# Kernel optimization log

Measured on AMD Instinct MI355X. Metric: run time of the kernel, lower is better.

Reference implementation:

```python
import jax, jax.numpy as jnp
import numpy as np

N = 50000      # nodes
E = 400000     # edges
IN = 128       # in_channels
C = 32         # out_channels per head
H1 = 8         # heads layer 1
MSG = 64       # msg_dim
TD = 64        # time encoder out_channels
ED = MSG + TD  # edge_dim = 128
HID = H1 * C   # 256


def _lin(k, fi, fo):
    return jax.random.normal(k, (fi, fo), jnp.float32) / np.float32(np.sqrt(fi))


def setup_inputs() -> dict:
    key = jax.random.key(0)
    ks = jax.random.split(key, 32)
    inp = {
        'x': jax.random.normal(ks[0], (N, IN), jnp.float32),
        'last_update': jax.random.uniform(ks[1], (N,), jnp.float32) * 1000.0,
        'edge_index': jax.random.randint(ks[2], (2, E), 0, N, jnp.int64),
        't': jax.random.uniform(ks[3], (E,), jnp.float32) * 1000.0,
        'msg': jax.random.normal(ks[4], (E, MSG), jnp.float32),
        # time encoder: Linear(1, TD) then cos
        'tw': jax.random.normal(ks[5], (TD,), jnp.float32),
        'tb': jnp.zeros((TD,), jnp.float32),
        # layer 1: TransformerConv(IN, C, heads=8, concat=True, edge_dim=ED)
        'Wq1': _lin(ks[6], IN, HID), 'bq1': jnp.zeros((HID,), jnp.float32),
        'Wk1': _lin(ks[7], IN, HID), 'bk1': jnp.zeros((HID,), jnp.float32),
        'Wv1': _lin(ks[8], IN, HID), 'bv1': jnp.zeros((HID,), jnp.float32),
        'We1': _lin(ks[9], ED, HID),                       # lin_edge, no bias
        'Ws1': _lin(ks[10], IN, HID), 'bs1': jnp.zeros((HID,), jnp.float32),
        # layer 2: TransformerConv(HID, C, heads=1, concat=False, edge_dim=ED)
        'Wq2': _lin(ks[11], HID, C), 'bq2': jnp.zeros((C,), jnp.float32),
        'Wk2': _lin(ks[12], HID, C), 'bk2': jnp.zeros((C,), jnp.float32),
        'Wv2': _lin(ks[13], HID, C), 'bv2': jnp.zeros((C,), jnp.float32),
        'We2': _lin(ks[14], ED, C),
        'Ws2': _lin(ks[15], HID, C), 'bs2': jnp.zeros((C,), jnp.float32),
    }
    return inp


def _seg_softmax(logits, seg, n):
    # numerically-stable softmax over variable-size neighborhoods (per dst node)
    m = jax.ops.segment_max(logits, seg, num_segments=n)
    m = jnp.where(jnp.isfinite(m), m, 0.0)
    e = jnp.exp(logits - jax.lax.stop_gradient(m)[seg])
    s = jax.ops.segment_sum(e, seg, num_segments=n)
    return e / (s[seg] + 1e-16)


def _transformer_conv(x, edge_attr, src, dst, Wq, bq, Wk, bk, Wv, bv, We, Ws, bs, heads, ch, concat):
    n = x.shape[0]
    q = (x @ Wq + bq).reshape(n, heads, ch)[dst]          # (E,H,C) gather at dst
    k = ((x @ Wk + bk)[src]).reshape(-1, heads, ch)       # (E,H,C) gather at src
    v = ((x @ Wv + bv)[src]).reshape(-1, heads, ch)
    e = (edge_attr @ We).reshape(-1, heads, ch)
    k = k + e
    alpha = (q * k).sum(-1) / np.float32(np.sqrt(ch))     # (E,H)
    alpha = _seg_softmax(alpha, dst, n)
    out = jax.ops.segment_sum(alpha[..., None] * (v + e), dst, num_segments=n)  # (N,H,C)
    out = out.reshape(n, heads * ch) if concat else out.mean(axis=1)
    return out + x @ Ws + bs                               # root/skip connection


def reference(x, last_update, edge_index, t, msg, tw, tb,
              Wq1, bq1, Wk1, bk1, Wv1, bv1, We1, Ws1, bs1,
              Wq2, bq2, Wk2, bk2, Wv2, bv2, We2, Ws2, bs2):
    src, dst = edge_index[0], edge_index[1]
    rel_t = last_update[src] - t                          # (E,)
    rel_enc = jnp.cos(rel_t[:, None] * tw[None, :] + tb)  # TGN time encoding (E,TD)
    edge_attr = jnp.concatenate([rel_enc, msg], axis=-1)  # (E,ED)
    h = jax.nn.relu(_transformer_conv(x, edge_attr, src, dst,
                                      Wq1, bq1, Wk1, bk1, Wv1, bv1, We1, Ws1, bs1,
                                      H1, C, True))
    out = jax.nn.relu(_transformer_conv(h, edge_attr, src, dst,
                                        Wq2, bq2, Wk2, bk2, Wv2, bv2, We2, Ws2, bs2,
                                        1, C, False))
    return out
```

## Files before the change

kernel.cpp:

```cpp
#include <hip/hip_runtime.h>
#include <math.h>

#define NN 50000
#define NE 400000
#define RSQRT32 0.17677669529663687f

typedef __attribute__((ext_vector_type(8))) short bf16x8;
typedef __attribute__((ext_vector_type(4))) float f32x4;
#define MFMA_B16(a, b, c) __builtin_amdgcn_mfma_f32_16x16x32_bf16(a, b, c, 0, 0, 0)

#define O_FLAG  0ULL
#define O_BSUM  256ULL
#define O_SRCI  1280ULL
#define O_DSTI  (O_SRCI + 1600000ULL)
#define O_DEG   (O_DSTI + 1600000ULL)
#define O_CUR   (O_DEG + 200192ULL)
#define O_START (O_CUR + 200192ULL)
#define O_SRCS  (O_START + 200704ULL)
#define O_ORIG  (O_SRCS + 1600000ULL)
#define O_RELT  (O_ORIG + 1600000ULL)
#define O_Q1    (O_RELT + 1600000ULL)
#define O_K1    (O_Q1 + 25600000ULL)
#define O_V1    (O_K1 + 25600000ULL)
#define O_S1M   (O_V1 + 25600000ULL)
#define O_G1    (O_S1M + 25600000ULL)
#define O_WB1   (O_G1 + 102400000ULL)
#define O_WG1   (O_WB1 + 262144ULL)
#define O_WF1   (O_WG1 + 65536ULL)
#define O_WB2   (O_WF1 + 65536ULL)
#define O_NUMV1 (O_WB2 + 65536ULL)
#define WS_TOTAL (O_NUMV1 + 51200000ULL)
#define O_S1    O_DSTI
#define O_A1    O_G1
#define O_H     O_V1
#define O_Q2    O_Q1
#define O_K2    (O_Q1 + 6400000ULL)
#define O_V2    (O_Q1 + 12800000ULL)
#define O_S2M   (O_Q1 + 19200000ULL)
#define O_G2    O_K1
#define O_A2    O_S1M
#define O_NUMV2 O_G1
#define O_S2    O_CUR

__device__ __forceinline__ unsigned short f2bf(float f) {
    unsigned int u = __float_as_uint(f);
    unsigned int r = (u + 0x7fffu + ((u >> 16) & 1u)) >> 16;
    return (unsigned short)r;
}
__device__ __forceinline__ float bf2f(unsigned short u) {
    return __uint_as_float(((unsigned int)u) << 16);
}
__device__ __forceinline__ float4 ld_bf16x4(const unsigned short* p) {
    const ushort4 u = *(const ushort4*)p;
    float4 r;
    r.x = bf2f(u.x); r.y = bf2f(u.y); r.z = bf2f(u.z); r.w = bf2f(u.w);
    return r;
}
__device__ __forceinline__ ushort4 st_bf16x4(float a, float b, float c, float d) {
    ushort4 u; u.x = f2bf(a); u.y = f2bf(b); u.z = f2bf(c); u.w = f2bf(d);
    return u;
}

__global__ void k_detect(const unsigned int* ei, int* flag) {
    if (threadIdx.x == 0) {
        int is64 = 1;
        for (int i = 0; i < 64; ++i)
            if (ei[2 * i + 1] != 0u) { is64 = 0; break; }
        *flag = is64;
    }
}

__global__ void k_convhist(const void* ei, const int* flag,
                           int* __restrict__ srcI, int* __restrict__ dstI,
                           int* __restrict__ deg) {
    int i = blockIdx.x * 256 + threadIdx.x;
    if (i >= NE) return;
    int s, d;
    if (*flag) {
        const long long* p = (const long long*)ei;
        s = (int)p[i]; d = (int)p[NE + i];
    } else {
        const int* p = (const int*)ei;
        s = p[i]; d = p[NE + i];
    }
    srcI[i] = s;
    dstI[i] = d;
    atomicAdd(&deg[d], 1);
}

__global__ void k_scanA(const int* __restrict__ deg, int* __restrict__ locs,
                        int* __restrict__ bsum) {
    __shared__ int sm[256];
    const int t = threadIdx.x;
    const int gidx = blockIdx.x * 256 + t;
    int v = (gidx < NN) ? deg[gidx] : 0;
    sm[t] = v;
    __syncthreads();
    for (int off = 1; off < 256; off <<= 1) {
        int u = (t >= off) ? sm[t - off] : 0;
        __syncthreads();
        sm[t] += u;
        __syncthreads();
    }
    if (gidx < NN) locs[gidx] = sm[t];
    if (t == 255) bsum[blockIdx.x] = sm[255];
}

__global__ void k_scanB(int* __restrict__ bsum) {
    __shared__ int sm[256];
    const int t = threadIdx.x;
    int v = (t < 196) ? bsum[t] : 0;
    sm[t] = v;
    __syncthreads();
    for (int off = 1; off < 256; off <<= 1) {
        int u = (t >= off) ? sm[t - off] : 0;
        __syncthreads();
        sm[t] += u;
        __syncthreads();
    }
    if (t < 196) bsum[t] = sm[t] - v;
}

__global__ void k_scanC(const int* __restrict__ deg, const int* __restrict__ bsum,
                        int* __restrict__ startA, int* __restrict__ cursor) {
    const int t = threadIdx.x;
    const int gidx = blockIdx.x * 256 + t;
    if (gidx < NN) {
        const int ex = startA[gidx] - deg[gidx] + bsum[blockIdx.x];
        startA[gidx] = ex;
        cursor[gidx] = ex;
    }
    if (gidx == 0) startA[NN] = NE;
}

__global__ void k_scatter(const int* __restrict__ srcI, const int* __restrict__ dstI,
                          const float* __restrict__ lu, const float* __restrict__ tE,
                          int* __restrict__ cursor,
                          int* __restrict__ srcS, int* __restrict__ orig,
                          float* __restrict__ relT) {
    int i = blockIdx.x * 256 + threadIdx.x;
    if (i >= NE) return;
    const int d = dstI[i];
    const int s = srcI[i];
    const int pos = atomicAdd(&cursor[d], 1);
    srcS[pos] = s;
    orig[pos] = i;
    relT[pos] = lu[s] - tE[i];
}

__global__ void k_prepw(
    const float* __restrict__ Wq1, const float* __restrict__ Wk1,
    const float* __restrict__ Wv1, const float* __restrict__ Ws1,
    const float* __restrict__ We1,
    const float* __restrict__ Wq2, const float* __restrict__ Wk2,
    const float* __restrict__ Wv2, const float* __restrict__ Ws2,
    unsigned short* __restrict__ WB1, unsigned short* __restrict__ WG1,
    unsigned short* __restrict__ WF1, unsigned short* __restrict__ WB2)
{
    const int i = blockIdx.x * 256 + threadIdx.x;
    if (i < 131072) {
        const int part = i >> 15;
        const int rem = i & 32767;
        const int n = rem >> 7, k = rem & 127;
        const float* W = part == 0 ? Wq1 : part == 1 ? Wk1 : part == 2 ? Wv1 : Ws1;
        WB1[i] = f2bf(W[(size_t)k * 256 + n]);
    } else if (i < 163840) {
        const int j = i - 131072;
        const int h = j >> 12, ko = (j >> 5) & 127, c = j & 31;
        WG1[j] = f2bf(We1[(size_t)ko * 256 + h * 32 + c]);
    } else if (i < 196608) {
        const int j = i - 163840;
        const int h = j >> 12, c = (j >> 7) & 31, ko = j & 127;
        WF1[j] = f2bf(We1[(size_t)ko * 256 + h * 32 + c]);
    } else if (i < 229376) {
        const int j = i - 196608;
        const int col = j >> 8, k = j & 255;
        const int part = col >> 5, pc = col & 31;
        const float* W = part == 0 ? Wq2 : part == 1 ? Wk2 : part == 2 ? Wv2 : Ws2;
        WB2[j] = f2bf(W[(size_t)k * 32 + pc]);
    }
}

__global__ __launch_bounds__(256) void k_gemm1m(
    const float* __restrict__ x, const unsigned short* __restrict__ WB1,
    const float* __restrict__ c0, const float* __restrict__ c1,
    const float* __restrict__ c2, const float* __restrict__ c3,
    unsigned short* __restrict__ Q1b, unsigned short* __restrict__ K1b,
    unsigned short* __restrict__ V1b, unsigned short* __restrict__ S1mb)
{
    __shared__ unsigned short As[64 * 136];
    __shared__ unsigned short Bs[64 * 136];
    const int t = threadIdx.x;
    const int row0 = blockIdx.x * 64;
    const int by = blockIdx.y;
    const int part = by >> 2;
    const int pcol0 = (by & 3) * 64;
    const float* bp = part == 0 ? c0 : part == 1 ? c1 : part == 2 ? c2 : c3;
    unsigned short* Ob = part == 0 ? Q1b : part == 1 ? K1b : part == 2 ? V1b : S1mb;

    {
        const int r = t >> 2, cc = (t & 3) * 32;
        const int gr = row0 + r;
        unsigned short* dst = As + r * 136 + cc;
        if (gr < NN) {
            const float4* xp = (const float4*)(x + (size_t)gr * 128 + cc);
            #pragma unroll
            for (int i = 0; i < 8; ++i) {
                const float4 v = xp[i];
                *(ushort4*)(dst + 4 * i) = st_bf16x4(v.x, v.y, v.z, v.w);
            }
        } else {
            const ushort4 z = {0, 0, 0, 0};
            #pragma unroll
            for (int i = 0; i < 8; ++i) *(ushort4*)(dst + 4 * i) = z;
        }
    }
    {
        const int n = t >> 2, kk = (t & 3) * 32;
        const unsigned short* src = WB1 + ((size_t)part * 256 + pcol0 + n) * 128 + kk;
        unsigned short* dst = Bs + n * 136 + kk;
        #pragma unroll
        for (int i = 0; i < 4; ++i)
            *(bf16x8*)(dst + 8 * i) = *(const bf16x8*)(src + 8 * i);
    }
    __syncthreads();

    const int w = t >> 6, lane = t & 63, m = lane & 15, quad = lane >> 4;
    f32x4 acc[4];
    #pragma unroll
    for (int i = 0; i < 4; ++i) acc[i] = (f32x4){0.f, 0.f, 0.f, 0.f};
    #pragma unroll
    for (int kc = 0; kc < 4; ++kc) {
        const bf16x8 af = *(const bf16x8*)(As + (16 * w + m) * 136 + kc * 32 + quad * 8);
        #pragma unroll
        for (int ct = 0; ct < 4; ++ct) {
            const bf16x8 bf = *(const bf16x8*)(Bs + (16 * ct + m) * 136 + kc * 32 + quad * 8);
            acc[ct] = MFMA_B16(af, bf, acc[ct]);
        }
    }
    #pragma unroll
    for (int ct = 0; ct < 4; ++ct) {
        const int colp = pcol0 + ct * 16 + m;
        const float b = bp[colp];
        #pragma unroll
        for (int r = 0; r < 4; ++r) {
            const int gr = row0 + 16 * w + quad * 4 + r;
            if (gr < NN) Ob[(size_t)gr * 256 + colp] = f2bf(acc[ct][r] + b);
        }
    }
}

__global__ __launch_bounds__(256) void k_g1m(
    const unsigned short* __restrict__ Q1b, const unsigned short* __restrict__ WG1,
    unsigned short* __restrict__ G1b)
{
    __shared__ unsigned short As[64 * 40];
    __shared__ unsigned short Bs[128 * 40];
    const int t = threadIdx.x;
    const int n0 = blockIdx.x * 64;
    const int h = blockIdx.y;
    {
        const int n = t >> 2, c = (t & 3) * 8;
        const int gn = n0 + n;
        bf16x8 v = {};
        if (gn < NN) v = *(const bf16x8*)(Q1b + (size_t)gn * 256 + h * 32 + c);
        *(bf16x8*)(As + n * 40 + c) = v;
    }
    {
        const int ko = t >> 1, c = (t & 1) * 16;
        const unsigned short* src = WG1 + (size_t)h * 4096 + ko * 32 + c;
        *(bf16x8*)(Bs + ko * 40 + c) = *(const bf16x8*)(src);
        *(bf16x8*)(Bs + ko * 40 + c + 8) = *(const bf16x8*)(src + 8);
    }
    __syncthreads();

    const int w = t >> 6, lane = t & 63, m = lane & 15, quad = lane >> 4;
    f32x4 acc[8];
    #pragma unroll
    for (int i = 0; i < 8; ++i) acc[i] = (f32x4){0.f, 0.f, 0.f, 0.f};
    const bf16x8 af = *(const bf16x8*)(As + (16 * w + m) * 40 + quad * 8);
    #pragma unroll
    for (int ct = 0; ct < 8; ++ct) {
        const bf16x8 bf = *(const bf16x8*)(Bs + (16 * ct + m) * 40 + quad * 8);
        acc[ct] = MFMA_B16(af, bf, acc[ct]);
    }
    #pragma unroll
    for (int ct = 0; ct < 8; ++ct) {
        const int k = ct * 16 + m;
        #pragma unroll
        for (int r = 0; r < 4; ++r) {
            const int gn = n0 + 16 * w + quad * 4 + r;
            if (gn < NN) G1b[(size_t)gn * 1024 + h * 128 + k] = f2bf(acc[ct][r]);
        }
    }
}

__global__ __launch_bounds__(256) void k_g2(
    const float* __restrict__ Q2, const float* __restrict__ We2,
    float* __restrict__ G2)
{
    __shared__ float Qs[64][36];
    __shared__ float Ws[128][36];
    const int t = threadIdx.x;
    const int n0 = blockIdx.x * 64;
    {
        const int n = t >> 2, c8 = (t & 3) * 8;
        float4 v0 = make_float4(0.f,0.f,0.f,0.f), v1 = v0;
        if (n0 + n < NN) {
            v0 = *(const float4*)(Q2 + (size_t)(n0 + n) * 32 + c8);
            v1 = *(const float4*)(Q2 + (size_t)(n0 + n) * 32 + c8 + 4);
        }
        *(float4*)(&Qs[n][c8]) = v0;
        *(float4*)(&Qs[n][c8 + 4]) = v1;
    }
    {
        const int k = t >> 1, c16 = (t & 1) * 16;
        #pragma unroll
        for (int i = 0; i < 4; ++i)
            *(float4*)(&Ws[k][c16 + 4 * i]) =
                *(const float4*)(We2 + (size_t)k * 32 + c16 + 4 * i);
    }
    __syncthreads();
    const int tx = t & 15, ty = t >> 4;
    const int k8 = tx * 8, n4 = ty * 4;
    float acc[4][8] = {};
    #pragma unroll 8
    for (int c = 0; c < 32; ++c) {
        float a[4], b[8];
        #pragma unroll
        for (int i = 0; i < 4; ++i) a[i] = Qs[n4 + i][c];
        #pragma unroll
        for (int j = 0; j < 8; ++j) b[j] = Ws[k8 + j][c];
        #pragma unroll
        for (int i = 0; i < 4; ++i)
            #pragma unroll
            for (int j = 0; j < 8; ++j)
                acc[i][j] += a[i] * b[j];
    }
    #pragma unroll
    for (int i = 0; i < 4; ++i) {
        const int gn = n0 + n4 + i;
        if (gn < NN) {
            float* gp = G2 + (size_t)gn * 128 + k8;
            *(float4*)(gp)     = make_float4(acc[i][0], acc[i][1], acc[i][2], acc[i][3]);
            *(float4*)(gp + 4) = make_float4(acc[i][4], acc[i][5], acc[i][6], acc[i][7]);
        }
    }
}

__global__ __launch_bounds__(256) __attribute__((amdgpu_waves_per_eu(3)))
void k_agg1(
    const int* __restrict__ startA, const int* __restrict__ srcS,
    const int* __restrict__ orig, const float* __restrict__ relT,
    const float* __restrict__ msg, const float* __restrict__ tw,
    const float* __restrict__ tb,
    const unsigned short* __restrict__ Q1b, const unsigned short* __restrict__ K1b,
    const unsigned short* __restrict__ V1b, const unsigned short* G1b,
    unsigned short* A1b, float* __restrict__ numv1, float* __restrict__ s1)
{
    const int t = threadIdx.x;
    const int g = t >> 5, l = t & 31;
    const int lane64 = t & 63;
    const int base32 = lane64 & 32;
    const int d = blockIdx.x * 8 + g;
    const int eb = startA[d], ee = startA[d + 1];
    const int hl = l >> 2;

    float q8[8];
    {
        const unsigned short* qp = Q1b + (size_t)d * 256 + l * 8;
        const float4 q0 = ld_bf16x4(qp), q1 = ld_bf16x4(qp + 4);
        q8[0]=q0.x; q8[1]=q0.y; q8[2]=q0.z; q8[3]=q0.w;
        q8[4]=q1.x; q8[5]=q1.y; q8[6]=q1.z; q8[7]=q1.w;
    }
    float gv[8][4];
    #pragma unroll
    for (int h = 0; h < 8; ++h) {
        const float4 gg = ld_bf16x4(G1b + (size_t)d * 1024 + h * 128 + l * 4);
        gv[h][0]=gg.x; gv[h][1]=gg.y; gv[h][2]=gg.z; gv[h][3]=gg.w;
    }
    float4 twl = make_float4(0.f,0.f,0.f,0.f), tbl = twl;
    if (l < 16) {
        twl = *(const float4*)(tw + l * 4);
        tbl = *(const float4*)(tb + l * 4);
    }

    float a1acc[8][4] = {};
    float nv[8] = {};
    float sacc = 0.f;

    const unsigned short* kbase = K1b + l * 8;
    const unsigned short* vbase = V1b + l * 8;

    bf16x8 kN = {}, vN = {};
    float aN[4] = {0.f, 0.f, 0.f, 0.f};

    #define PREF1(EIDX) {                                                     \
        const int s_ = srcS[EIDX];                                            \
        if (l < 16) {                                                         \
            const float rt_ = relT[EIDX];                                     \
            aN[0] = __cosf(rt_ * twl.x + tbl.x);                              \
            aN[1] = __cosf(rt_ * twl.y + tbl.y);                              \
            aN[2] = __cosf(rt_ * twl.z + tbl.z);                              \
            aN[3] = __cosf(rt_ * twl.w + tbl.w);                              \
        } else {                                                              \
            const float4 m4_ = *(const float4*)(msg + (size_t)orig[EIDX] * 64 \
                                                + (l - 16) * 4);              \
            aN[0]=m4_.x; aN[1]=m4_.y; aN[2]=m4_.z; aN[3]=m4_.w;               \
        }                                                                     \
        kN = *(const bf16x8*)(kbase + (size_t)s_ * 256);                      \
        vN = *(const bf16x8*)(vbase + (size_t)s_ * 256);                      \
    }

    if (eb < ee) PREF1(eb);

    for (int e = eb; e < ee; ++e) {
        const bf16x8 kc = kN, vc = vN;
        const float a0 = aN[0], a1 = aN[1], a2 = aN[2], a3 = aN[3];
        if (e + 1 < ee) PREF1(e + 1);

        float part[8];
        #pragma unroll
        for (int h = 0; h < 8; ++h)
            part[h] = a0*gv[h][0] + a1*gv[h][1] + a2*gv[h][2] + a3*gv[h][3];
        {
            float kf[8];
            #pragma unroll
            for (int i = 0; i < 8; ++i) kf[i] = bf2f((unsigned short)kc[i]);
            part[hl] += q8[0]*kf[0] + q8[1]*kf[1] + q8[2]*kf[2] + q8[3]*kf[3]
                      + q8[4]*kf[4] + q8[5]*kf[5] + q8[6]*kf[6] + q8[7]*kf[7];
        }

        float t4[4];
        {
            const bool b = (l & 1) != 0;
            #pragma unroll
            for (int i = 0; i < 4; ++i) {
                const float give = b ? part[i] : part[4 + i];
                const float keep = b ? part[4 + i] : part[i];
                t4[i] = keep + __shfl_xor(give, 1);
            }
        }
        float t2[2];
        {
            const bool b = (l & 2) != 0;
            #pragma unroll
            for (int i = 0; i < 2; ++i) {
                const float give = b ? t4[i] : t4[2 + i];
                const float keep = b ? t4[2 + i] : t4[i];
                t2[i] = keep + __shfl_xor(give, 2);
            }
        }
        float t1;
        {
            const bool b = (l & 4) != 0;
            const float give = b ? t2[0] : t2[1];
            const float keep = b ? t2[1] : t2[0];
            t1 = keep + __shfl_xor(give, 4);
        }
        t1 += __shfl_xor(t1, 8);
        t1 += __shfl_xor(t1, 16);

        const float pe = __expf(fminf(t1 * RSQRT32, 80.f));
        float p_all[8];
        p_all[0] = __shfl(pe, base32 + 0);
        p_all[1] = __shfl(pe, base32 + 4);
        p_all[2] = __shfl(pe, base32 + 2);
        p_all[3] = __shfl(pe, base32 + 6);
        p_all[4] = __shfl(pe, base32 + 1);
        p_all[5] = __shfl(pe, base32 + 5);
        p_all[6] = __shfl(pe, base32 + 3);
        p_all[7] = __shfl(pe, base32 + 7);

        #pragma unroll
        for (int h = 0; h < 8; ++h) {
            a1acc[h][0] += p_all[h]*a0; a1acc[h][1] += p_all[h]*a1;
            a1acc[h][2] += p_all[h]*a2; a1acc[h][3] += p_all[h]*a3;
        }
        {
            float vf[8];
            #pragma unroll
            for (int i = 0; i < 8; ++i) vf[i] = bf2f((unsigned short)vc[i]);
            const float pv = p_all[hl];
            nv[0] += pv*vf[0]; nv[1] += pv*vf[1]; nv[2] += pv*vf[2]; nv[3] += pv*vf[3];
            nv[4] += pv*vf[4]; nv[5] += pv*vf[5]; nv[6] += pv*vf[6]; nv[7] += pv*vf[7];
            sacc += pv;
        }
    }
    #undef PREF1

    #pragma unroll
    for (int h = 0; h < 8; ++h)
        *(ushort4*)(A1b + (size_t)d * 1024 + h * 128 + l * 4) =
            st_bf16x4(a1acc[h][0], a1acc[h][1], a1acc[h][2], a1acc[h][3]);
    float* np = numv1 + (size_t)d * 256 + l * 8;
    *(float4*)(np)     = make_float4(nv[0], nv[1], nv[2], nv[3]);
    *(float4*)(np + 4) = make_float4(nv[4], nv[5], nv[6], nv[7]);
    if ((l & 3) == 0) s1[(size_t)d * 8 + hl] = sacc;
}

__global__ __launch_bounds__(256) void k_foldC1m(
    const unsigned short* __restrict__ A1b, const unsigned short* __restrict__ WF1,
    const float* __restrict__ numv1, const float* __restrict__ s1,
    const unsigned short* __restrict__ S1mb, unsigned short* __restrict__ hb)
{
    __shared__ unsigned short As[64 * 136];
    __shared__ unsigned short Bs[32 * 136];
    const int t = threadIdx.x;
    const int n0 = blockIdx.x * 64;
    const int h = blockIdx.y;
    {
        const int n = t >> 2, kk = (t & 3) * 32;
        const int gn = n0 + n;
        unsigned short* dst = As + n * 136 + kk;
        if (gn < NN) {
            const unsigned short* src = A1b + (size_t)gn * 1024 + h * 128 + kk;
            #pragma unroll
            for (int i = 0; i < 4; ++i)
                *(bf16x8*)(dst + 8 * i) = *(const bf16x8*)(src + 8 * i);
        } else {
            const bf16x8 z = {};
            #pragma unroll
            for (int i = 0; i < 4; ++i) *(bf16x8*)(dst + 8 * i) = z;
        }
    }
    {
        const int c = t >> 3, kk = (t & 7) * 16;
        const unsigned short* src = WF1 + (size_t)h * 4096 + c * 128 + kk;
        *(bf16x8*)(Bs + c * 136 + kk) = *(const bf16x8*)(src);
        *(bf16x8*)(Bs + c * 136 + kk + 8) = *(const bf16x8*)(src + 8);
    }
    __syncthreads();

    const int w = t >> 6, lane = t & 63, m = lane & 15, quad = lane >> 4;
    f32x4 acc[2];
    acc[0] = (f32x4){0.f, 0.f, 0.f, 0.f};
    acc[1] = (f32x4){0.f, 0.f, 0.f, 0.f};
    #pragma unroll
    for (int kc = 0; kc < 4; ++kc) {
        const bf16x8 af = *(const bf16x8*)(As + (16 * w + m) * 136 + kc * 32 + quad * 8);
        #pragma unroll
        for (int ct = 0; ct < 2; ++ct) {
            const bf16x8 bf = *(const bf16x8*)(Bs + (16 * ct + m) * 136 + kc * 32 + quad * 8);
            acc[ct] = MFMA_B16(af, bf, acc[ct]);
        }
    }
    #pragma unroll
    for (int ct = 0; ct < 2; ++ct) {
        const int c = ct * 16 + m;
        #pragma unroll
        for (int r = 0; r < 4; ++r) {
            const int gn = n0 + 16 * w + quad * 4 + r;
            if (gn < NN) {
                const float s = s1[(size_t)gn * 8 + h] + 1e-16f;
                const float nvv = numv1[(size_t)gn * 256 + h * 32 + c];
                const float sk = bf2f(S1mb[(size_t)gn * 256 + h * 32 + c]);
                float v = (acc[ct][r] + nvv) / s + sk;
                v = v > 0.f ? v : 0.f;
                hb[(size_t)gn * 256 + h * 32 + c] = f2bf(v);
            }
        }
    }
}

__global__ __launch_bounds__(256) void k_gemm2m(
    const unsigned short* __restrict__ hb, const unsigned short* __restrict__ WB2,
    const float* __restrict__ c0, const float* __restrict__ c1,
    const float* __restrict__ c2, const float* __restrict__ c3,
    float* __restrict__ O0, float* __restrict__ O1,
    float* __restrict__ O2, float* __restrict__ O3)
{
    __shared__ unsigned short As[64 * 136];
    __shared__ unsigned short Bs[64 * 136];
    const int t = threadIdx.x;
    const int row0 = blockIdx.x * 64;
    const int coly = blockIdx.y;
    const int w = t >> 6, lane = t & 63, m = lane & 15, quad = lane >> 4;

    f32x4 acc[4];
    #pragma unroll
    for (int i = 0; i < 4; ++i) acc[i] = (f32x4){0.f, 0.f, 0.f, 0.f};

    for (int kb = 0; kb < 2; ++kb) {
        if (kb) __syncthreads();
        {
            const int r = t >> 2, kk = (t & 3) * 32;
            const int gr = row0 + r;
            unsigned short* dst = As + r * 136 + kk;
            if (gr < NN) {
                const unsigned short* src = hb + (size_t)gr * 256 + kb * 128 + kk;
                #pragma unroll
                for (int i = 0; i < 4; ++i)
                    *(bf16x8*)(dst + 8 * i) = *(const bf16x8*)(src + 8 * i);
            } else {
                const bf16x8 z = {};
                #pragma unroll
                for (int i = 0; i < 4; ++i) *(bf16x8*)(dst + 8 * i) = z;
            }
        }
        {
            const int n = t >> 2, kk = (t & 3) * 32;
            const unsigned short* src = WB2 + (size_t)(coly * 64 + n) * 256 + kb * 128 + kk;
            unsigned short* dst = Bs + n * 136 + kk;
            #pragma unroll
            for (int i = 0; i < 4; ++i)
                *(bf16x8*)(dst + 8 * i) = *(const bf16x8*)(src + 8 * i);
        }
        __syncthreads();
        #pragma unroll
        for (int kc = 0; kc < 4; ++kc) {
            const bf16x8 af = *(const bf16x8*)(As + (16 * w + m) * 136 + kc * 32 + quad * 8);
            #pragma unroll
            for (int ct = 0; ct < 4; ++ct) {
                const bf16x8 bf = *(const bf16x8*)(Bs + (16 * ct + m) * 136 + kc * 32 + quad * 8);
                acc[ct] = MFMA_B16(af, bf, acc[ct]);
            }
        }
    }
    #pragma unroll
    for (int ct = 0; ct < 4; ++ct) {
        const int col = coly * 64 + ct * 16 + m;
        const int part = col >> 5, pc = col & 31;
        const float* bb = part == 0 ? c0 : part == 1 ? c1 : part == 2 ? c2 : c3;
        float* Op = part == 0 ? O0 : part == 1 ? O1 : part == 2 ? O2 : O3;
        const float b = bb[pc];
        #pragma unroll
        for (int r = 0; r < 4; ++r) {
            const int gr = row0 + 16 * w + quad * 4 + r;
            if (gr < NN) Op[(size_t)gr * 32 + pc] = acc[ct][r] + b;
        }
    }
}

__global__ __launch_bounds__(256) void k_aggB2(
    const int* __restrict__ startA, const int* __restrict__ srcS,
    const int* __restrict__ orig, const float* __restrict__ relT,
    const float* __restrict__ msg, const float* __restrict__ tw,
    const float* __restrict__ tb,
    const float* __restrict__ Q2, const float* __restrict__ K2,
    const float* __restrict__ V2, const float* __restrict__ G2,
    float* __restrict__ A2, float* __restrict__ numv2, float* __restrict__ s2)
{
    const int t = threadIdx.x;
    const int g = t >> 5, l = t & 31;
    const int d = blockIdx.x * 8 + g;
    const int eb = startA[d], ee = startA[d + 1];

    const float q2l = Q2[(size_t)d * 32 + l];
    const float4 g2l = *(const float4*)(G2 + (size_t)d * 128 + l * 4);
    float4 twl = make_float4(0.f,0.f,0.f,0.f), tbl = twl;
    if (l < 16) {
        twl = *(const float4*)(tw + l * 4);
        tbl = *(const float4*)(tb + l * 4);
    }
    float acc2[4] = {};
    float nvacc = 0.f, sacc = 0.f;

    float kNv = 0.f, vNv = 0.f;
    float aN[4] = {0.f, 0.f, 0.f, 0.f};

    #define PREF2(EIDX) {                                                     \
        const int s_ = srcS[EIDX];                                            \
        kNv = K2[(size_t)s_ * 32 + l];                                        \
        vNv = V2[(size_t)s_ * 32 + l];                                        \
        if (l < 16) {                                                         \
            const float rt_ = relT[EIDX];                                     \
            aN[0] = __cosf(rt_ * twl.x + tbl.x);                              \
            aN[1] = __cosf(rt_ * twl.y + tbl.y);                              \
            aN[2] = __cosf(rt_ * twl.z + tbl.z);                              \
            aN[3] = __cosf(rt_ * twl.w + tbl.w);                              \
        } else {                                                              \
            const float4 m4_ = *(const float4*)(msg + (size_t)orig[EIDX] * 64 \
                                                + (l - 16) * 4);              \
            aN[0]=m4_.x; aN[1]=m4_.y; aN[2]=m4_.z; aN[3]=m4_.w;               \
        }                                                                     \
    }

    if (eb < ee) PREF2(eb);

    for (int e = eb; e < ee; ++e) {
        const float kc = kNv, vcv = vNv;
        const float a0 = aN[0], a1 = aN[1], a2 = aN[2], a3 = aN[3];
        if (e + 1 < ee) PREF2(e + 1);

        float part = q2l * kc;
        part += a0 * g2l.x + a1 * g2l.y + a2 * g2l.z + a3 * g2l.w;
        part += __shfl_xor(part, 1);
        part += __shfl_xor(part, 2);
        part += __shfl_xor(part, 4);
        part += __shfl_xor(part, 8);
        part += __shfl_xor(part, 16);
        const float p = __expf(fminf(part * RSQRT32, 80.f));
        acc2[0] += p * a0; acc2[1] += p * a1;
        acc2[2] += p * a2; acc2[3] += p * a3;
        nvacc += p * vcv;
        sacc += p;
    }
    #undef PREF2

    *(float4*)(A2 + (size_t)d * 128 + l * 4) =
        make_float4(acc2[0], acc2[1], acc2[2], acc2[3]);
    numv2[(size_t)d * 32 + l] = nvacc;
    if (l == 0) s2[d] = sacc;
}

__global__ __launch_bounds__(256) void k_foldC2(
    const float* __restrict__ A2, const float* __restrict__ We2,
    const float* __restrict__ numv2, const float* __restrict__ s2,
    const float* __restrict__ S2m, float* __restrict__ out)
{
    __shared__ float Ws[128][36];
    const int t = threadIdx.x;
    {
        const int k = t >> 1, c16 = (t & 1) * 16;
        #pragma unroll
        for (int i = 0; i < 4; ++i)
            *(float4*)(&Ws[k][c16 + 4 * i]) =
                *(const float4*)(We2 + (size_t)k * 32 + c16 + 4 * i);
    }
    __syncthreads();
    const int n = blockIdx.x * 8 + (t >> 5);
    const int c = t & 31;
    const float* ap = A2 + (size_t)n * 128;
    float acc = 0.f;
    #pragma unroll 8
    for (int k = 0; k < 128; k += 4) {
        const float4 a4 = *(const float4*)(ap + k);
        acc += a4.x * Ws[k][c] + a4.y * Ws[k + 1][c] +
               a4.z * Ws[k + 2][c] + a4.w * Ws[k + 3][c];
    }
    const float s = s2[n] + 1e-16f;
    float v = (numv2[(size_t)n * 32 + c] + acc) / s + S2m[(size_t)n * 32 + c];
    out[(size_t)n * 32 + c] = v > 0.f ? v : 0.f;
}

extern "C" void kernel_launch(void* const* d_in, const int* in_sizes, int n_in,
                              void* d_out, int out_size, void* d_ws, size_t ws_size,
                              hipStream_t stream) {
    const float* x   = (const float*)d_in[0];
    const float* lu  = (const float*)d_in[1];
    const void*  ei  = d_in[2];
    const float* tE  = (const float*)d_in[3];
    const float* msg = (const float*)d_in[4];
    const float* tw  = (const float*)d_in[5];
    const float* tb  = (const float*)d_in[6];
    const float* Wq1 = (const float*)d_in[7];  const float* bq1 = (const float*)d_in[8];
    const float* Wk1 = (const float*)d_in[9];  const float* bk1 = (const float*)d_in[10];
    const float* Wv1 = (const float*)d_in[11]; const float* bv1 = (const float*)d_in[12];
    const float* We1 = (const float*)d_in[13];
    const float* Ws1 = (const float*)d_in[14]; const float* bs1 = (const float*)d_in[15];
    const float* Wq2 = (const float*)d_in[16]; const float* bq2 = (const float*)d_in[17];
    const float* Wk2 = (const float*)d_in[18]; const float* bk2 = (const float*)d_in[19];
    const float* Wv2 = (const float*)d_in[20]; const float* bv2 = (const float*)d_in[21];
    const float* We2 = (const float*)d_in[22];
    const float* Ws2 = (const float*)d_in[23]; const float* bs2 = (const float*)d_in[24];
    float* out = (float*)d_out;
    char* ws = (char*)d_ws;

    if (ws_size < WS_TOTAL) return;

    int* flag   = (int*)(ws + O_FLAG);
    int* bsum   = (int*)(ws + O_BSUM);
    int* srcI   = (int*)(ws + O_SRCI);
    int* dstI   = (int*)(ws + O_DSTI);
    int* deg    = (int*)(ws + O_DEG);
    int* cursor = (int*)(ws + O_CUR);
    int* startA = (int*)(ws + O_START);
    int* srcS   = (int*)(ws + O_SRCS);
    int* orig   = (int*)(ws + O_ORIG);
    float* relT = (float*)(ws + O_RELT);
    unsigned short* Q1b  = (unsigned short*)(ws + O_Q1);
    unsigned short* K1b  = (unsigned short*)(ws + O_K1);
    unsigned short* V1b  = (unsigned short*)(ws + O_V1);
    unsigned short* S1mb = (unsigned short*)(ws + O_S1M);
    unsigned short* G1b  = (unsigned short*)(ws + O_G1);
    unsigned short* A1b  = (unsigned short*)(ws + O_A1);
    float* numv1 = (float*)(ws + O_NUMV1);
    float* s1    = (float*)(ws + O_S1);
    unsigned short* hb = (unsigned short*)(ws + O_H);
    float* Q2   = (float*)(ws + O_Q2);
    float* K2m  = (float*)(ws + O_K2);
    float* V2m  = (float*)(ws + O_V2);
    float* S2m  = (float*)(ws + O_S2M);
    float* G2   = (float*)(ws + O_G2);
    float* A2   = (float*)(ws + O_A2);
    float* numv2 = (float*)(ws + O_NUMV2);
    float* s2   = (float*)(ws + O_S2);
    unsigned short* WB1 = (unsigned short*)(ws + O_WB1);
    unsigned short* WG1 = (unsigned short*)(ws + O_WG1);
    unsigned short* WF1 = (unsigned short*)(ws + O_WF1);
    unsigned short* WB2 = (unsigned short*)(ws + O_WB2);

    hipMemsetAsync(ws + O_DEG, 0, 200000, stream);

    k_detect<<<1, 64, 0, stream>>>((const unsigned int*)ei, flag);
    k_convhist<<<(NE + 255) / 256, 256, 0, stream>>>(ei, flag, srcI, dstI, deg);
    k_scanA<<<196, 256, 0, stream>>>(deg, startA, bsum);
    k_scanB<<<1, 256, 0, stream>>>(bsum);
    k_scanC<<<196, 256, 0, stream>>>(deg, bsum, startA, cursor);
    k_scatter<<<(NE + 255) / 256, 256, 0, stream>>>(srcI, dstI, lu, tE, cursor,
                                                    srcS, orig, relT);
    k_prepw<<<896, 256, 0, stream>>>(Wq1, Wk1, Wv1, Ws1, We1, Wq2, Wk2, Wv2, Ws2,
                                     WB1, WG1, WF1, WB2);
    k_gemm1m<<<dim3(782, 16), 256, 0, stream>>>(
        x, WB1, bq1, bk1, bv1, bs1, Q1b, K1b, V1b, S1mb);
    k_g1m<<<dim3(782, 8), 256, 0, stream>>>(Q1b, WG1, G1b);
    k_agg1<<<NN / 8, 256, 0, stream>>>(startA, srcS, orig, relT, msg, tw, tb,
                                       Q1b, K1b, V1b, G1b, A1b, numv1, s1);
    k_foldC1m<<<dim3(782, 8), 256, 0, stream>>>(A1b, WF1, numv1, s1, S1mb, hb);
    k_gemm2m<<<dim3(782, 2), 256, 0, stream>>>(
        hb, WB2, bq2, bk2, bv2, bs2, Q2, K2m, V2m, S2m);
    k_g2<<<782, 256, 0, stream>>>(Q2, We2, G2);
    k_aggB2<<<NN / 8, 256, 0, stream>>>(startA, srcS, orig, relT, msg, tw, tb,
                                        Q2, K2m, V2m, G2, A2, numv2, s2);
    k_foldC2<<<NN / 8, 256, 0, stream>>>(A2, We2, numv2, s2, S2m, out);
}
```

Before: 807.4 us.

## Batch edge index loads per warp chunk and deepen gather prefetch in aggregation kernels

Both edge-aggregation kernels now load the src, relT and orig indices for up to 32 edges at once, one per lane, and broadcast them with shuffles. This removes the serial dependent index load that preceded each gather. The gather prefetch is also deepened from one edge to two in flight, and cos is computed at use time instead of at prefetch time. k_aggB2 gets a waves-per-EU hint of 4. In exchange, more registers hold prefetched data and extra shuffles are spent per edge, which may lower occupancy in k_agg1.

Result: faster. 754.9 us (-6.5%).

```diff
diff --git a/kernel.cpp b/kernel.cpp
--- a/kernel.cpp
+++ b/kernel.cpp
@@ -360,8 +360,7 @@
 {
     const int t = threadIdx.x;
     const int g = t >> 5, l = t & 31;
-    const int lane64 = t & 63;
-    const int base32 = lane64 & 32;
+    const int base32 = (t & 63) & 32;
     const int d = blockIdx.x * 8 + g;
     const int eb = startA[d], ee = startA[d + 1];
     const int hl = l >> 2;
@@ -392,102 +391,123 @@
     const unsigned short* kbase = K1b + l * 8;
     const unsigned short* vbase = V1b + l * 8;
 
-    bf16x8 kN = {}, vN = {};
-    float aN[4] = {0.f, 0.f, 0.f, 0.f};
-
-    #define PREF1(EIDX) {                                                     \
-        const int s_ = srcS[EIDX];                                            \
-        if (l < 16) {                                                         \
-            const float rt_ = relT[EIDX];                                     \
-            aN[0] = __cosf(rt_ * twl.x + tbl.x);                              \
-            aN[1] = __cosf(rt_ * twl.y + tbl.y);                              \
-            aN[2] = __cosf(rt_ * twl.z + tbl.z);                              \
-            aN[3] = __cosf(rt_ * twl.w + tbl.w);                              \
-        } else {                                                              \
-            const float4 m4_ = *(const float4*)(msg + (size_t)orig[EIDX] * 64 \
-                                                + (l - 16) * 4);              \
-            aN[0]=m4_.x; aN[1]=m4_.y; aN[2]=m4_.z; aN[3]=m4_.w;               \
-        }                                                                     \
-        kN = *(const bf16x8*)(kbase + (size_t)s_ * 256);                      \
-        vN = *(const bf16x8*)(vbase + (size_t)s_ * 256);                      \
-    }
-
-    if (eb < ee) PREF1(eb);
-
-    for (int e = eb; e < ee; ++e) {
-        const bf16x8 kc = kN, vc = vN;
-        const float a0 = aN[0], a1 = aN[1], a2 = aN[2], a3 = aN[3];
-        if (e + 1 < ee) PREF1(e + 1);
-
-        float part[8];
-        #pragma unroll
-        for (int h = 0; h < 8; ++h)
-            part[h] = a0*gv[h][0] + a1*gv[h][1] + a2*gv[h][2] + a3*gv[h][3];
-        {
-            float kf[8];
+    for (int c = eb; c < ee; c += 32) {
+        const int cnt = (ee - c < 32) ? (ee - c) : 32;
+        const bool lvld = (c + l) < ee;
+        const int   sv = lvld ? srcS[c + l] : 0;
+        const float rv = lvld ? relT[c + l] : 0.f;
+        const int   ov = lvld ? orig[c + l] : 0;
+
+        bf16x8 kA = {}, vA = {}, kB = {}, vB = {};
+        float4 mA = make_float4(0.f,0.f,0.f,0.f), mB = mA;
+        float  rA = 0.f, rB = 0.f;
+
+        auto issue = [&](int jj, bf16x8& kD, bf16x8& vD, float4& mD, float& rD) {
+            const int s_ = __shfl(sv, base32 + jj);
+            rD = __shfl(rv, base32 + jj);
+            const int o_ = __shfl(ov, base32 + jj);
+            kD = *(const bf16x8*)(kbase + (size_t)s_ * 256);
+            vD = *(const bf16x8*)(vbase + (size_t)s_ * 256);
+            if (l >= 16)
+                mD = *(const float4*)(msg + (size_t)o_ * 64 + (l - 16) * 4);
+        };
+
+        auto body = [&](const bf16x8 kc, const bf16x8 vc, const float4 mc,
+                        const float rc) {
+            float a0, a1, a2, a3;
+            if (l < 16) {
+                a0 = __cosf(rc * twl.x + tbl.x);
+                a1 = __cosf(rc * twl.y + tbl.y);
+                a2 = __cosf(rc * twl.z + tbl.z);
+                a3 = __cosf(rc * twl.w + tbl.w);
+            } else {
+                a0 = mc.x; a1 = mc.y; a2 = mc.z; a3 = mc.w;
+            }
+            float part[8];
             #pragma unroll
-            for (int i = 0; i < 8; ++i) kf[i] = bf2f((unsigned short)kc[i]);
-            part[hl] += q8[0]*kf[0] + q8[1]*kf[1] + q8[2]*kf[2] + q8[3]*kf[3]
-                      + q8[4]*kf[4] + q8[5]*kf[5] + q8[6]*kf[6] + q8[7]*kf[7];
-        }
-
-        float t4[4];
-        {
-            const bool b = (l & 1) != 0;
+            for (int h = 0; h < 8; ++h)
+                part[h] = a0*gv[h][0] + a1*gv[h][1] + a2*gv[h][2] + a3*gv[h][3];
+            {
+                float kf[8];
+                #pragma unroll
+                for (int i = 0; i < 8; ++i) kf[i] = bf2f((unsigned short)kc[i]);
+                part[hl] += q8[0]*kf[0] + q8[1]*kf[1] + q8[2]*kf[2] + q8[3]*kf[3]
+                          + q8[4]*kf[4] + q8[5]*kf[5] + q8[6]*kf[6] + q8[7]*kf[7];
+            }
+            float t4[4];
+            {
+                const bool b = (l & 1) != 0;
+                #pragma unroll
+                for (int i = 0; i < 4; ++i) {
+                    const float give = b ? part[i] : part[4 + i];
+                    const float keep = b ? part[4 + i] : part[i];
+                    t4[i] = keep + __shfl_xor(give, 1);
+                }
+            }
+            float t2[2];
+            {
+                const bool b = (l & 2) != 0;
+                #pragma unroll
+                for (int i = 0; i < 2; ++i) {
+                    const float give = b ? t4[i] : t4[2 + i];
+                    const float keep = b ? t4[2 + i] : t4[i];
+                    t2[i] = keep + __shfl_xor(give, 2);
+                }
+            }
+            float t1;
+            {
+                const bool b = (l & 4) != 0;
+                const float give = b ? t2[0] : t2[1];
+                const float keep = b ? t2[1] : t2[0];
+                t1 = keep + __shfl_xor(give, 4);
+            }
+            t1 += __shfl_xor(t1, 8);
+            t1 += __shfl_xor(t1, 16);
+
+            const float pe = __expf(fminf(t1 * RSQRT32, 80.f));
+            float p_all[8];
+            p_all[0] = __shfl(pe, base32 + 0);
+            p_all[1] = __shfl(pe, base32 + 4);
+            p_all[2] = __shfl(pe, base32 + 2);
+            p_all[3] = __shfl(pe, base32 + 6);
+            p_all[4] = __shfl(pe, base32 + 1);
+            p_all[5] = __shfl(pe, base32 + 5);
+            p_all[6] = __shfl(pe, base32 + 3);
+            p_all[7] = __shfl(pe, base32 + 7);
+
             #pragma unroll
-            for (int i = 0; i < 4; ++i) {
-                const float give = b ? part[i] : part[4 + i];
-                const float keep = b ? part[4 + i] : part[i];
-                t4[i] = keep + __shfl_xor(give, 1);
-            }
-        }
-        float t2[2];
-        {
-            const bool b = (l & 2) != 0;
-            #pragma unroll
-            for (int i = 0; i < 2; ++i) {
-                const float give = b ? t4[i] : t4[2 + i];
-                const float keep = b ? t4[2 + i] : t4[i];
-                t2[i] = keep + __shfl_xor(give, 2);
-            }
-        }
-        float t1;
-        {
-            const bool b = (l & 4) != 0;
-            const float give = b ? t2[0] : t2[1];
-            const float keep = b ? t2[1] : t2[0];
-            t1 = keep + __shfl_xor(give, 4);
-        }
-        t1 += __shfl_xor(t1, 8);
-        t1 += __shfl_xor(t1, 16);
-
-        const float pe = __expf(fminf(t1 * RSQRT32, 80.f));
-        float p_all[8];
-        p_all[0] = __shfl(pe, base32 + 0);
-        p_all[1] = __shfl(pe, base32 + 4);
-        p_all[2] = __shfl(pe, base32 + 2);
-        p_all[3] = __shfl(pe, base32 + 6);
-        p_all[4] = __shfl(pe, base32 + 1);
-        p_all[5] = __shfl(pe, base32 + 5);
-        p_all[6] = __shfl(pe, base32 + 3);
-        p_all[7] = __shfl(pe, base32 + 7);
-
-        #pragma unroll
-        for (int h = 0; h < 8; ++h) {
-            a1acc[h][0] += p_all[h]*a0; a1acc[h][1] += p_all[h]*a1;
-            a1acc[h][2] += p_all[h]*a2; a1acc[h][3] += p_all[h]*a3;
-        }
-        {
-            float vf[8];
-            #pragma unroll
-            for (int i = 0; i < 8; ++i) vf[i] = bf2f((unsigned short)vc[i]);
-            const float pv = p_all[hl];
-            nv[0] += pv*vf[0]; nv[1] += pv*vf[1]; nv[2] += pv*vf[2]; nv[3] += pv*vf[3];
-            nv[4] += pv*vf[4]; nv[5] += pv*vf[5]; nv[6] += pv*vf[6]; nv[7] += pv*vf[7];
-            sacc += pv;
-        }
-    }
-    #undef PREF1
+            for (int h = 0; h < 8; ++h) {
+                a1acc[h][0] += p_all[h]*a0; a1acc[h][1] += p_all[h]*a1;
+                a1acc[h][2] += p_all[h]*a2; a1acc[h][3] += p_all[h]*a3;
+            }
+            {
+                float vf[8];
+                #pragma unroll
+                for (int i = 0; i < 8; ++i) vf[i] = bf2f((unsigned short)vc[i]);
+                const float pv = p_all[hl];
+                nv[0] += pv*vf[0]; nv[1] += pv*vf[1]; nv[2] += pv*vf[2]; nv[3] += pv*vf[3];
+                nv[4] += pv*vf[4]; nv[5] += pv*vf[5]; nv[6] += pv*vf[6]; nv[7] += pv*vf[7];
+                sacc += pv;
+            }
+        };
+
+        if (cnt > 0) issue(0, kA, vA, mA, rA);
+        if (cnt > 1) issue(1, kB, vB, mB, rB);
+        for (int j = 0; j < cnt; j += 2) {
+            {
+                const bf16x8 kc = kA, vc = vA;
+                const float4 mc = mA; const float rc = rA;
+                if (j + 2 < cnt) issue(j + 2, kA, vA, mA, rA);
+                body(kc, vc, mc, rc);
+            }
+            if (j + 1 < cnt) {
+                const bf16x8 kc = kB, vc = vB;
+                const float4 mc = mB; const float rc = rB;
+                if (j + 3 < cnt) issue(j + 3, kB, vB, mB, rB);
+                body(kc, vc, mc, rc);
+            }
+        }
+    }
 
     #pragma unroll
     for (int h = 0; h < 8; ++h)
@@ -632,7 +652,8 @@
     }
 }
 
-__global__ __launch_bounds__(256) void k_aggB2(
+__global__ __launch_bounds__(256) __attribute__((amdgpu_waves_per_eu(4)))
+void k_aggB2(
     const int* __restrict__ startA, const int* __restrict__ srcS,
     const int* __restrict__ orig, const float* __restrict__ relT,
     const float* __restrict__ msg, const float* __restrict__ tw,
@@ -643,6 +664,7 @@
 {
     const int t = threadIdx.x;
     const int g = t >> 5, l = t & 31;
+    const int base32 = (t & 63) & 32;
     const int d = blockIdx.x * 8 + g;
     const int eb = startA[d], ee = startA[d + 1];
 
@@ -656,47 +678,67 @@
     float acc2[4] = {};
     float nvacc = 0.f, sacc = 0.f;
 
-    float kNv = 0.f, vNv = 0.f;
-    float aN[4] = {0.f, 0.f, 0.f, 0.f};
-
-    #define PREF2(EIDX) {                                                     \
-        const int s_ = srcS[EIDX];                                            \
-        kNv = K2[(size_t)s_ * 32 + l];                                        \
-        vNv = V2[(size_t)s_ * 32 + l];                                        \
-        if (l < 16) {                                                         \
-            const float rt_ = relT[EIDX];                                     \
-            aN[0] = __cosf(rt_ * twl.x + tbl.x);                              \
-            aN[1] = __cosf(rt_ * twl.y + tbl.y);                              \
-            aN[2] = __cosf(rt_ * twl.z + tbl.z);                              \
-            aN[3] = __cosf(rt_ * twl.w + tbl.w);                              \
-        } else {                                                              \
-            const float4 m4_ = *(const float4*)(msg + (size_t)orig[EIDX] * 64 \
-                                                + (l - 16) * 4);              \
-            aN[0]=m4_.x; aN[1]=m4_.y; aN[2]=m4_.z; aN[3]=m4_.w;               \
-        }                                                                     \
-    }
-
-    if (eb < ee) PREF2(eb);
-
-    for (int e = eb; e < ee; ++e) {
-        const float kc = kNv, vcv = vNv;
-        const float a0 = aN[0], a1 = aN[1], a2 = aN[2], a3 = aN[3];
-        if (e + 1 < ee) PREF2(e + 1);
-
-        float part = q2l * kc;
-        part += a0 * g2l.x + a1 * g2l.y + a2 * g2l.z + a3 * g2l.w;
-        part += __shfl_xor(part, 1);
-        part += __shfl_xor(part, 2);
-        part += __shfl_xor(part, 4);
-        part += __shfl_xor(part, 8);
-        part += __shfl_xor(part, 16);
-        const float p = __expf(fminf(part * RSQRT32, 80.f));
-        acc2[0] += p * a0; acc2[1] += p * a1;
-        acc2[2] += p * a2; acc2[3] += p * a3;
-        nvacc += p * vcv;
-        sacc += p;
-    }
-    #undef PREF2
+    for (int c = eb; c < ee; c += 32) {
+        const int cnt = (ee - c < 32) ? (ee - c) : 32;
+        const bool lvld = (c + l) < ee;
+        const int   sv = lvld ? srcS[c + l] : 0;
+        const float rv = lvld ? relT[c + l] : 0.f;
+        const int   ov = lvld ? orig[c + l] : 0;
+
+        float kA = 0.f, vA = 0.f, kB = 0.f, vB = 0.f, rA = 0.f, rB = 0.f;
+        float4 mA = make_float4(0.f,0.f,0.f,0.f), mB = mA;
+
+        auto issue = [&](int jj, float& kD, float& vD, float4& mD, float& rD) {
+            const int s_ = __shfl(sv, base32 + jj);
+            rD = __shfl(rv, base32 + jj);
+            const int o_ = __shfl(ov, base32 + jj);
+            kD = K2[(size_t)s_ * 32 + l];
+            vD = V2[(size_t)s_ * 32 + l];
+            if (l >= 16)
+                mD = *(const float4*)(msg + (size_t)o_ * 64 + (l - 16) * 4);
+        };
+        auto body = [&](const float kc, const float vcv, const float4 mc,
+                        const float rc) {
+            float a0, a1, a2, a3;
+            if (l < 16) {
+                a0 = __cosf(rc * twl.x + tbl.x);
+                a1 = __cosf(rc * twl.y + tbl.y);
+                a2 = __cosf(rc * twl.z + tbl.z);
+                a3 = __cosf(rc * twl.w + tbl.w);
+            } else {
+                a0 = mc.x; a1 = mc.y; a2 = mc.z; a3 = mc.w;
+            }
+            float part = q2l * kc;
+            part += a0 * g2l.x + a1 * g2l.y + a2 * g2l.z + a3 * g2l.w;
+            part += __shfl_xor(part, 1);
+            part += __shfl_xor(part, 2);
+            part += __shfl_xor(part, 4);
+            part += __shfl_xor(part, 8);
+            part += __shfl_xor(part, 16);
+            const float p = __expf(fminf(part * RSQRT32, 80.f));
+            acc2[0] += p * a0; acc2[1] += p * a1;
+            acc2[2] += p * a2; acc2[3] += p * a3;
+            nvacc += p * vcv;
+            sacc += p;
+        };
+
+        if (cnt > 0) issue(0, kA, vA, mA, rA);
+        if (cnt > 1) issue(1, kB, vB, mB, rB);
+        for (int j = 0; j < cnt; j += 2) {
+            {
+                const float kc = kA, vcv = vA;
+                const float4 mc = mA; const float rc = rA;
+                if (j + 2 < cnt) issue(j + 2, kA, vA, mA, rA);
+                body(kc, vcv, mc, rc);
+            }
+            if (j + 1 < cnt) {
+                const float kc = kB, vcv = vB;
+                const float4 mc = mB; const float rc = rB;
+                if (j + 3 < cnt) issue(j + 3, kB, vB, mB, rB);
+                body(kc, vcv, mc, rc);
+            }
+        }
+    }
 
     *(float4*)(A2 + (size_t)d * 128 + l * 4) =
         make_float4(acc2[0], acc2[1], acc2[2], acc2[3]);
```
